# Performance work log

Measured on AMD Instinct MI355X. Metric: run time of the kernel, lower is better.

## Reference

```python
import jax, jax.numpy as jnp
import numpy as np

# static config (matches init_kwargs / chosen grid)
T, H, W = 8, 32, 32          # video token grid
WT, WH, WW = 4, 8, 8         # swin window
HEADS, HD = 16, 128
DIM = HEADS * HD             # 2048
LT = 256                     # text length
EPS = 1e-6
NT, NH, NW_ = T // WT, H // WH, W // WW
NWIN = NT * NH * NW_
WLEN = WT * WH * WW


def rmsnorm(x, g):
    # x: [..., HD], g: [HD]
    var = jnp.mean(x * x, axis=-1, keepdims=True)
    return x * jax.lax.rsqrt(var + EPS) * g


def setup_inputs() -> dict:
    key = jax.random.key(0)
    ks = jax.random.split(key, 8)
    s = 0.02
    Lv = T * H * W
    return {
        'vid': jax.random.normal(ks[0], (Lv, DIM), jnp.float32),
        'txt': jax.random.normal(ks[1], (LT, DIM), jnp.float32),
        'Wqkv_v': jax.random.normal(ks[2], (DIM, 3 * DIM), jnp.float32) * s,
        'bqkv_v': jnp.zeros((3 * DIM,), jnp.float32),
        'Wqkv_t': jax.random.normal(ks[3], (DIM, 3 * DIM), jnp.float32) * s,
        'bqkv_t': jnp.zeros((3 * DIM,), jnp.float32),
        'Wo_v': jax.random.normal(ks[4], (DIM, DIM), jnp.float32) * s,
        'bo_v': jnp.zeros((DIM,), jnp.float32),
        'Wo_t': jax.random.normal(ks[5], (DIM, DIM), jnp.float32) * s,
        'bo_t': jnp.zeros((DIM,), jnp.float32),
        'gq_v': jnp.ones((HD,), jnp.float32),
        'gk_v': jnp.ones((HD,), jnp.float32),
        'gq_t': jnp.ones((HD,), jnp.float32),
        'gk_t': jnp.ones((HD,), jnp.float32),
    }


def _forward(vid, txt, Wqkv_v, bqkv_v, Wqkv_t, bqkv_t, Wo_v, bo_v, Wo_t, bo_t,
             gq_v, gk_v, gq_t, gk_t):
    # per-modality QKV projections
    vqkv = vid @ Wqkv_v + bqkv_v                      # [Lv, 3*DIM]
    tqkv = txt @ Wqkv_t + bqkv_t                      # [LT, 3*DIM]
    # swin window partition: [T,H,W,C] -> [nWin, WLEN, 3, h, d]
    x = vqkv.reshape(NT, WT, NH, WH, NW_, WW, 3 * DIM)
    x = x.transpose(0, 2, 4, 1, 3, 5, 6).reshape(NWIN, WLEN, 3, HEADS, HD)
    vq, vk, vv = x[:, :, 0], x[:, :, 1], x[:, :, 2]
    t = tqkv.reshape(LT, 3, HEADS, HD)
    tq, tk, tv = t[:, 0], t[:, 1], t[:, 2]
    # QK norm (per-head RMSNorm with affine)
    vq, vk = rmsnorm(vq, gq_v), rmsnorm(vk, gk_v)
    tq, tk = rmsnorm(tq, gq_t), rmsnorm(tk, gk_t)
    # concat full text to every window (repeat_concat_idx)
    bt = lambda a: jnp.broadcast_to(a[None], (NWIN,) + a.shape)
    q = jnp.concatenate([vq, bt(tq)], axis=1)          # [nWin, S, h, d]
    k = jnp.concatenate([vk, bt(tk)], axis=1)
    v = jnp.concatenate([vv, bt(tv)], axis=1)
    # attention within each window (flash-varlen equivalent, equal lengths)
    scale = 1.0 / np.sqrt(HD).astype(np.float32)
    scores = jnp.einsum('nqhd,nkhd->nhqk', q, k) * scale
    p = jax.nn.softmax(scores, axis=-1)
    o = jnp.einsum('nhqk,nkhd->nqhd', p, v)            # [nWin, S, h, d]
    vo = o[:, :WLEN].reshape(NWIN, WLEN, DIM)
    to = o[:, WLEN:].mean(axis=0).reshape(LT, DIM)     # un-repeat text: mean over windows
    # window reverse -> flat [Lv, DIM]
    vo = vo.reshape(NT, NH, NW_, WT, WH, WW, DIM)
    vo = vo.transpose(0, 3, 1, 4, 2, 5, 6).reshape(T * H * W, DIM)
    return (vo @ Wo_v + bo_v, to @ Wo_t + bo_t)


def reference(vid, txt, Wqkv_v, bqkv_v, Wqkv_t, bqkv_t, Wo_v, bo_v, Wo_t, bo_t,
              gq_v, gk_v, gq_t, gk_t):
    return _forward(vid, txt, Wqkv_v, bqkv_v, Wqkv_t, bqkv_t, Wo_v, bo_v,
                    Wo_t, bo_t, gq_v, gk_v, gq_t, gk_t)
```

## Files before the change

### kernel.cpp

```cpp
#include <hip/hip_runtime.h>

typedef unsigned short u16;
typedef unsigned int   u32;
typedef __attribute__((ext_vector_type(8))) short short8;
typedef __attribute__((ext_vector_type(4))) float f32x4;

__device__ __forceinline__ u16 f2bf(float f) {
  union { float f; u32 u; } v; v.f = f;
  u32 r = v.u + 0x7fffu + ((v.u >> 16) & 1u);
  return (u16)(r >> 16);
}
__device__ __forceinline__ float bf2f(u32 bits) {
  union { u32 u; float f; } v; v.u = bits << 16; return v.f;
}
__device__ __forceinline__ void gl_lds16(const u16* g, u16* l) {
  __builtin_amdgcn_global_load_lds(
      (const __attribute__((address_space(1))) void*)g,
      (__attribute__((address_space(3))) void*)l, 16, 0, 0);
}

static constexpr int DIM  = 2048;
static constexpr int NQKV = 6144;

__global__ __launch_bounds__(256) void conv_f32_bf16(const float* __restrict__ in,
                                                     u16* __restrict__ out, int n4) {
  int id = blockIdx.x * 256 + threadIdx.x;
  if (id >= n4) return;
  float4 v = ((const float4*)in)[id];
  u32 lo = (u32)f2bf(v.x) | ((u32)f2bf(v.y) << 16);
  u32 hi = (u32)f2bf(v.z) | ((u32)f2bf(v.w) << 16);
  ((uint2*)out)[id] = make_uint2(lo, hi);
}

__global__ void tconv_kernel(const float* __restrict__ W, u16* __restrict__ Wt, int K, int N) {
  __shared__ float t[32][33];
  int tx = threadIdx.x, ty = threadIdx.y;
  int n0 = blockIdx.x * 32, k0 = blockIdx.y * 32;
  #pragma unroll
  for (int i = 0; i < 4; ++i)
    t[ty + i*8][tx] = W[(size_t)(k0 + ty + i*8) * N + n0 + tx];
  __syncthreads();
  #pragma unroll
  for (int i = 0; i < 4; ++i)
    Wt[(size_t)(n0 + ty + i*8) * K + k0 + tx] = f2bf(t[tx][ty + i*8]);
}

__global__ __launch_bounds__(256) void rms_kernel(u16* __restrict__ x,
                                                  const float* __restrict__ g, int nrows) {
  int w = threadIdx.x >> 6, lane = threadIdx.x & 63;
  int rid = blockIdx.x * 4 + w;
  if (rid >= nrows) return;
  u32* row = (u32*)x + (size_t)rid * 64;
  u32 u = row[lane];
  float f0 = bf2f(u & 0xffffu), f1 = bf2f(u >> 16);
  float s = f0*f0 + f1*f1;
  #pragma unroll
  for (int off = 1; off <= 32; off <<= 1) s += __shfl_xor(s, off);
  float r = rsqrtf(s * (1.0f/128.0f) + 1e-6f);
  float g0 = g[lane*2], g1 = g[lane*2+1];
  row[lane] = (u32)f2bf(f0*r*g0) | ((u32)f2bf(f1*r*g1) << 16);
}

__global__ __launch_bounds__(256)
void vtrans_kernel(const u16* __restrict__ src, u16* __restrict__ dst) {
  __shared__ u16 t[64][130];
  int nh = blockIdx.x, k0 = blockIdx.y * 64;
  const u16* s = src + ((size_t)nh*256 + k0)*128;
  u16* d = dst + (size_t)nh*128*256 + k0;
  int tid = threadIdx.x;
  #pragma unroll
  for (int it = 0; it < 4; ++it) {
    int c = tid + it*256;
    int row = c >> 4, ch = c & 15;
    short8 v = *(const short8*)(s + row*128 + ch*8);
    u32* dst32 = (u32*)&t[row][ch*8];
    const u32* v32 = (const u32*)&v;
    dst32[0] = v32[0]; dst32[1] = v32[1]; dst32[2] = v32[2]; dst32[3] = v32[3];
  }
  __syncthreads();
  #pragma unroll
  for (int it = 0; it < 4; ++it) {
    int c = tid + it*256;
    int dr = c >> 3, kg = c & 7;
    short8 v;
    #pragma unroll
    for (int j = 0; j < 8; ++j) v[j] = (short)t[kg*8+j][dr];
    *(short8*)(d + (size_t)dr*256 + kg*8) = v;
  }
}

template<int EPI>
__global__ __launch_bounds__(512, 2)
void gemm256(const u16* __restrict__ A, const u16* __restrict__ Bt,
             const float* __restrict__ bias,
             u16* __restrict__ o0, u16* __restrict__ o1, u16* __restrict__ o2,
             float* __restrict__ of, int ldo, int M, int N, int K)
{
  __shared__ __align__(16) u16 As[4][256*32];
  __shared__ __align__(16) u16 Bs[4][256*32];
  const int NT = K >> 5;
  int tid = threadIdx.x, lane = tid & 63, w = tid >> 6;
  int l15 = lane & 15, l4 = lane >> 4;
  int wm = w >> 2, wn = w & 3;

  int nbx = gridDim.x;
  int nwg = nbx * gridDim.y;
  int bid = blockIdx.y * nbx + blockIdx.x;
  int cpx = nwg >> 3;
  int swz = (bid & 7) * cpx + (bid >> 3);
  int n0 = (swz % nbx) * 256, m0 = (swz / nbx) * 256;

  int srow = tid >> 2, skc = (tid & 3) ^ ((tid >> 3) & 3);
  const u16* aS = A  + (size_t)(m0 + srow) * K + skc * 8;
  const u16* bS = Bt + (size_t)(n0 + srow) * K + skc * 8;
  const size_t halfStride = 128 * (size_t)K;
  const int ldsBase = w * 512;

  #define STAGE_A(slot, tt, half) \
    gl_lds16(aS + (size_t)(tt)*32 + (half)*halfStride, &As[slot][(half)*4096 + ldsBase])
  #define STAGE_B(slot, tt, half) \
    gl_lds16(bS + (size_t)(tt)*32 + (half)*halfStride, &Bs[slot][(half)*4096 + ldsBase])

  #pragma unroll
  for (int pt = 0; pt < 3; ++pt) {
    STAGE_A(pt, pt, 0); STAGE_A(pt, pt, 1);
    STAGE_B(pt, pt, 0); STAGE_B(pt, pt, 1);
  }
  asm volatile("s_waitcnt vmcnt(8)" ::: "memory");
  __builtin_amdgcn_s_barrier();

  f32x4 acc[8][4] = {};

  for (int t = 0; t < NT; ++t) {
    const u16* ab = As[t & 3];
    const u16* bb = Bs[t & 3];
    bool st = (t + 3 < NT);
    int slot = (t + 3) & 3;

    short8 bf_[4], af[4];
    #pragma unroll
    for (int j = 0; j < 4; ++j) {
      int rb = wn*64 + j*16 + l15;
      bf_[j] = *(const short8*)((const char*)bb + rb*64 + ((l4 ^ ((rb>>1)&3))*16));
    }
    #pragma unroll
    for (int i = 0; i < 4; ++i) {
      int ra = wm*128 + i*16 + l15;
      af[i] = *(const short8*)((const char*)ab + ra*64 + ((l4 ^ ((ra>>1)&3))*16));
    }
    if (st) { STAGE_A(slot, t+3, 0); STAGE_A(slot, t+3, 1); }
    __builtin_amdgcn_s_barrier();
    asm volatile("s_waitcnt lgkmcnt(0)" ::: "memory");
    __builtin_amdgcn_sched_barrier(0);
    __builtin_amdgcn_s_setprio(1);
    #pragma unroll
    for (int i = 0; i < 4; ++i)
      #pragma unroll
      for (int j = 0; j < 4; ++j)
        acc[i][j] = __builtin_amdgcn_mfma_f32_16x16x32_bf16(af[i], bf_[j], acc[i][j], 0, 0, 0);
    __builtin_amdgcn_s_setprio(0);
    __builtin_amdgcn_s_barrier();

    #pragma unroll
    for (int i = 0; i < 4; ++i) {
      int ra = wm*128 + 64 + i*16 + l15;
      af[i] = *(const short8*)((const char*)ab + ra*64 + ((l4 ^ ((ra>>1)&3))*16));
    }
    if (st) { STAGE_B(slot, t+3, 0); STAGE_B(slot, t+3, 1); }
    __builtin_amdgcn_s_barrier();
    asm volatile("s_waitcnt lgkmcnt(0)" ::: "memory");
    __builtin_amdgcn_sched_barrier(0);
    __builtin_amdgcn_s_setprio(1);
    #pragma unroll
    for (int i = 0; i < 4; ++i)
      #pragma unroll
      for (int j = 0; j < 4; ++j)
        acc[4+i][j] = __builtin_amdgcn_mfma_f32_16x16x32_bf16(af[i], bf_[j], acc[4+i][j], 0, 0, 0);
    __builtin_amdgcn_s_setprio(0);
    if (t <= NT - 4)      asm volatile("s_waitcnt vmcnt(8)" ::: "memory");
    else if (t == NT - 3) asm volatile("s_waitcnt vmcnt(4)" ::: "memory");
    else if (t == NT - 2) asm volatile("s_waitcnt vmcnt(0)" ::: "memory");
    __builtin_amdgcn_s_barrier();
  }
  #undef STAGE_A
  #undef STAGE_B

  #pragma unroll
  for (int i = 0; i < 8; ++i)
    #pragma unroll
    for (int j = 0; j < 4; ++j)
      #pragma unroll
      for (int r = 0; r < 4; ++r) {
        int m = m0 + wm*128 + i*16 + l4*4 + r;
        int n = n0 + wn*64  + j*16 + l15;
        float v = acc[i][j][r] + bias[n];
        if (EPI == 0) {
          int which = n >> 11, head = (n >> 7) & 15, d = n & 127;
          int t = m >> 10, hh = (m >> 5) & 31, ww = m & 31;
          int win = ((t>>2)<<4) + ((hh>>3)<<2) + (ww>>3);
          int p   = ((t&3)<<6) + ((hh&7)<<3) + (ww&7);
          u16* dst = which == 0 ? o0 : (which == 1 ? o1 : o2);
          dst[((size_t)(win*16 + head)*256 + p)*128 + d] = f2bf(v);
        } else {
          of[(size_t)m * ldo + n] = v;
        }
      }
}

template<int EPI>
__global__ __launch_bounds__(256)
void gemm128(const u16* __restrict__ A, const u16* __restrict__ Bt,
             const float* __restrict__ bias,
             u16* __restrict__ o0, u16* __restrict__ o1, u16* __restrict__ o2,
             float* __restrict__ of, int ldo, int M, int N, int K)
{
  __shared__ __align__(16) u16 As[128*32];
  __shared__ __align__(16) u16 Bs[128*32];
  int tid = threadIdx.x, lane = tid & 63, w = tid >> 6;
  int l15 = lane & 15, l4 = lane >> 4;
  int m0 = blockIdx.y * 128, n0 = blockIdx.x * 128;
  int wr = (w >> 1) * 64, wc = (w & 1) * 64;
  f32x4 acc[4][4] = {};

  int o0b = (w    )*1024 + lane*16;
  int o1b = (w + 4)*1024 + lane*16;
  int r0 = o0b >> 6, c0 = ((o0b >> 4) & 3) ^ ((r0 >> 1) & 3);
  int r1 = o1b >> 6, c1 = ((o1b >> 4) & 3) ^ ((r1 >> 1) & 3);
  const u16* a0 = A  + (size_t)(m0 + r0)*K + c0*8;
  const u16* a1 = A  + (size_t)(m0 + r1)*K + c1*8;
  const u16* b0 = Bt + (size_t)(n0 + r0)*K + c0*8;
  const u16* b1 = Bt + (size_t)(n0 + r1)*K + c1*8;
  u16* dA0 = As + (w    )*512;
  u16* dA1 = As + (w + 4)*512;
  u16* dB0 = Bs + (w    )*512;
  u16* dB1 = Bs + (w + 4)*512;

  for (int k0 = 0; k0 < K; k0 += 32) {
    gl_lds16(a0 + k0, dA0);
    gl_lds16(a1 + k0, dA1);
    gl_lds16(b0 + k0, dB0);
    gl_lds16(b1 + k0, dB1);
    __syncthreads();
    short8 af[4], bfr[4];
    #pragma unroll
    for (int t = 0; t < 4; ++t) {
      int ra = wr + t*16 + l15;
      af[t]  = *(const short8*)((const char*)As + ra*64 + ((l4 ^ ((ra>>1)&3))*16));
      int rb = wc + t*16 + l15;
      bfr[t] = *(const short8*)((const char*)Bs + rb*64 + ((l4 ^ ((rb>>1)&3))*16));
    }
    #pragma unroll
    for (int i = 0; i < 4; ++i)
      #pragma unroll
      for (int j = 0; j < 4; ++j)
        acc[i][j] = __builtin_amdgcn_mfma_f32_16x16x32_bf16(af[i], bfr[j], acc[i][j], 0, 0, 0);
    __syncthreads();
  }

  #pragma unroll
  for (int i = 0; i < 4; ++i)
    #pragma unroll
    for (int j = 0; j < 4; ++j)
      #pragma unroll
      for (int r = 0; r < 4; ++r) {
        int m = m0 + wr + i*16 + l4*4 + r;
        int n = n0 + wc + j*16 + l15;
        float v = acc[i][j][r] + bias[n];
        if (EPI == 1) {
          int which = n >> 11, head = (n >> 7) & 15, d = n & 127;
          u16* dst = which == 0 ? o0 : (which == 1 ? o1 : o2);
          dst[((size_t)head*256 + m)*128 + d] = f2bf(v);
        } else {
          of[(size_t)m * ldo + n] = v;
        }
      }
}

__global__ __launch_bounds__(512)
void attn_kernel(const u16* __restrict__ vq, const u16* __restrict__ vk, const u16* __restrict__ vv,
                 const u16* __restrict__ tq, const u16* __restrict__ tk, const u16* __restrict__ tv,
                 const float* __restrict__ gq_v, const float* __restrict__ gq_t,
                 u16* __restrict__ vo, float* __restrict__ to_acc)
{
  __shared__ __align__(16) u16 Ks[64*128];
  __shared__ __align__(16) u16 Vt[128*64];
  __shared__ __align__(16) u16 Ps[8][16*80];
  int tid = threadIdx.x, lane = tid & 63, w = tid >> 6;
  int l15 = lane & 15, l4 = lane >> 4;
  int bid = blockIdx.x;
  int logical = (bid & 7) * 256 + (bid >> 3);
  int nh_ = logical >> 2, qq = logical & 3;
  int h = nh_ & 15;
  int n = nh_ >> 4;
  int qt = qq * 128 + w * 16;

  const u16* Qb; const float* gq;
  if (qt < 256) { Qb = vq + ((size_t)nh_*256 + qt)*128; gq = gq_v; }
  else          { Qb = tq + ((size_t)h  *256 + (qt-256))*128; gq = gq_t; }
  short8 qf[4];
  float qv[4][8];
  float ss = 0.f;
  #pragma unroll
  for (int dt = 0; dt < 4; ++dt) {
    qf[dt] = *(const short8*)(Qb + l15*128 + l4*8 + dt*32);
    #pragma unroll
    for (int j = 0; j < 8; ++j) {
      float f = bf2f((u16)qf[dt][j]);
      qv[dt][j] = f; ss += f*f;
    }
  }
  ss += __shfl_xor(ss, 16); ss += __shfl_xor(ss, 32);
  float rr = rsqrtf(ss * (1.0f/128.0f) + 1e-6f);
  #pragma unroll
  for (int dt = 0; dt < 4; ++dt) {
    float4 g0 = *(const float4*)(gq + l4*8 + dt*32);
    float4 g1 = *(const float4*)(gq + l4*8 + dt*32 + 4);
    qf[dt][0] = (short)f2bf(qv[dt][0]*rr*g0.x); qf[dt][1] = (short)f2bf(qv[dt][1]*rr*g0.y);
    qf[dt][2] = (short)f2bf(qv[dt][2]*rr*g0.z); qf[dt][3] = (short)f2bf(qv[dt][3]*rr*g0.w);
    qf[dt][4] = (short)f2bf(qv[dt][4]*rr*g1.x); qf[dt][5] = (short)f2bf(qv[dt][5]*rr*g1.y);
    qf[dt][6] = (short)f2bf(qv[dt][6]*rr*g1.z); qf[dt][7] = (short)f2bf(qv[dt][7]*rr*g1.w);
  }

  int oK0 = w*1024 + lane*16, oK1 = oK0 + 8192;
  int kr0 = oK0 >> 8, kc0 = ((oK0 >> 4) & 15) ^ (kr0 & 7);
  int kr1 = oK1 >> 8, kc1 = ((oK1 >> 4) & 15) ^ (kr1 & 7);
  int vd0 = oK0 >> 7, vc0 = ((oK0 >> 4) & 7) ^ (vd0 & 7);
  int vd1 = oK1 >> 7, vc1 = ((oK1 >> 4) & 7) ^ (vd1 & 7);
  u16* KD0 = Ks + (w*1024)/2;  u16* KD1 = Ks + (w*1024 + 8192)/2;
  u16* VD0 = Vt + (w*1024)/2;  u16* VD1 = Vt + (w*1024 + 8192)/2;

  f32x4 o_[8] = {};
  float m_run[4] = {-1e30f,-1e30f,-1e30f,-1e30f};
  float l_run[4] = {0.f,0.f,0.f,0.f};
  const float scale = 0.08838834764831845f;
  u16* pb = Ps[w];

  for (int c = 0; c < 8; ++c) {
    int kb = c * 64;
    const u16* Kc; const u16* Vb; int vkb;
    if (kb < 256) { Kc = vk + ((size_t)nh_*256 + kb)*128; Vb = vv + (size_t)nh_*128*256; vkb = kb; }
    else          { Kc = tk + ((size_t)h  *256 + (kb-256))*128; Vb = tv + (size_t)h*128*256; vkb = kb - 256; }
    gl_lds16(Kc + kr0*128 + kc0*8, KD0);
    gl_lds16(Kc + kr1*128 + kc1*8, KD1);
    gl_lds16(Vb + (size_t)vd0*256 + vkb + vc0*8, VD0);
    gl_lds16(Vb + (size_t)vd1*256 + vkb + vc1*8, VD1);
    __syncthreads();

    f32x4 s4[4];
    __builtin_amdgcn_s_setprio(1);
    #pragma unroll
    for (int kt = 0; kt < 4; ++kt) {
      f32x4 sa = {0.f,0.f,0.f,0.f};
      int key = kt*16 + l15;
      #pragma unroll
      for (int dt = 0; dt < 4; ++dt) {
        int c16b = l4 + dt*4;
        short8 kf = *(const short8*)((const char*)Ks + key*256 + (((c16b ^ (key&7)))*16));
        sa = __builtin_amdgcn_mfma_f32_16x16x32_bf16(qf[dt], kf, sa, 0, 0, 0);
      }
      s4[kt] = sa;
    }
    __builtin_amdgcn_s_setprio(0);

    float f_[4];
    #pragma unroll
    for (int r = 0; r < 4; ++r) {
      float mx = fmaxf(fmaxf(s4[0][r], s4[1][r]), fmaxf(s4[2][r], s4[3][r])) * scale;
      #pragma unroll
      for (int off = 1; off <= 8; off <<= 1) mx = fmaxf(mx, __shfl_xor(mx, off));
      float nm = fmaxf(m_run[r], mx);
      f_[r] = __expf(m_run[r] - nm);
      m_run[r] = nm;
    }
    float p[4][4];
    #pragma unroll
    for (int kt = 0; kt < 4; ++kt)
      #pragma unroll
      for (int r = 0; r < 4; ++r)
        p[kt][r] = __expf(s4[kt][r]*scale - m_run[r]);
    #pragma unroll
    for (int r = 0; r < 4; ++r) {
      float sum = p[0][r] + p[1][r] + p[2][r] + p[3][r];
      #pragma unroll
      for (int off = 1; off <= 8; off <<= 1) sum += __shfl_xor(sum, off);
      l_run[r] = l_run[r]*f_[r] + sum;
    }
    #pragma unroll
    for (int dt = 0; dt < 8; ++dt) {
      f32x4 t = o_[dt];
      t[0]*=f_[0]; t[1]*=f_[1]; t[2]*=f_[2]; t[3]*=f_[3];
      o_[dt] = t;
    }

    #pragma unroll
    for (int kt = 0; kt < 4; ++kt)
      #pragma unroll
      for (int r = 0; r < 4; ++r)
        pb[(l4*4 + r)*80 + kt*16 + l15] = f2bf(p[kt][r]);
    #pragma unroll
    for (int ks = 0; ks < 2; ++ks) {
      short8 pa = *(const short8*)((const char*)pb + l15*160 + ks*64 + l4*16);
      __builtin_amdgcn_s_setprio(1);
      #pragma unroll
      for (int dt = 0; dt < 8; ++dt) {
        int d = dt*16 + l15;
        short8 vf = *(const short8*)((const char*)Vt + d*128 + (((ks*4 + l4) ^ (d&7))<<4));
        o_[dt] = __builtin_amdgcn_mfma_f32_16x16x32_bf16(pa, vf, o_[dt], 0, 0, 0);
      }
      __builtin_amdgcn_s_setprio(0);
    }
    __syncthreads();
  }

  float inv[4];
  #pragma unroll
  for (int r = 0; r < 4; ++r) inv[r] = 1.0f / l_run[r];
  int nt = n >> 4, nh2 = (n >> 2) & 3, nw = n & 3;
  #pragma unroll
  for (int dt = 0; dt < 8; ++dt) {
    int d = dt*16 + l15;
    int col = h*128 + d;
    #pragma unroll
    for (int r = 0; r < 4; ++r) {
      float val = o_[dt][r] * inv[r];
      int q = qt + l4*4 + r;
      if (q < 256) {
        int wt = q >> 6, wh = (q >> 3) & 7, ww = q & 7;
        int rg = ((nt*4 + wt)*32 + (nh2*8 + wh))*32 + (nw*8 + ww);
        vo[(size_t)rg*2048 + col] = f2bf(val);
      } else {
        atomicAdd(to_acc + (size_t)(q - 256)*2048 + col, val * (1.0f/32.0f));
      }
    }
  }
}

extern "C" void kernel_launch(void* const* d_in, const int* in_sizes, int n_in,
                              void* d_out, int out_size, void* d_ws, size_t ws_size,
                              hipStream_t stream) {
  const float* vid    = (const float*)d_in[0];
  const float* txt    = (const float*)d_in[1];
  const float* Wqkv_v = (const float*)d_in[2];
  const float* bqkv_v = (const float*)d_in[3];
  const float* Wqkv_t = (const float*)d_in[4];
  const float* bqkv_t = (const float*)d_in[5];
  const float* Wo_v   = (const float*)d_in[6];
  const float* bo_v   = (const float*)d_in[7];
  const float* Wo_t   = (const float*)d_in[8];
  const float* bo_t   = (const float*)d_in[9];
  const float* gq_v   = (const float*)d_in[10];
  const float* gk_v   = (const float*)d_in[11];
  const float* gq_t   = (const float*)d_in[12];
  const float* gk_t   = (const float*)d_in[13];
  float* out = (float*)d_out;

  char* p = (char*)d_ws;
  u16* vid_bf   = (u16*)p;  p += 8192ull*2048*2;
  u16* txt_bf   = (u16*)p;  p += 256ull*2048*2;
  u16* Wqkv_v_t = (u16*)p;  p += 6144ull*2048*2;
  u16* Wqkv_t_t = (u16*)p;  p += 6144ull*2048*2;
  u16* Wo_v_t   = (u16*)p;  p += 2048ull*2048*2;
  u16* Wo_t_t   = (u16*)p;  p += 2048ull*2048*2;
  u16* vq_w     = (u16*)p;  p += 32ull*16*256*128*2;
  u16* vk_w     = (u16*)p;  p += 32ull*16*256*128*2;
  u16* vv_w     = (u16*)p;  p += 32ull*16*256*128*2;
  u16* tq_w     = (u16*)p;  p += 16ull*256*128*2;
  u16* tk_w     = (u16*)p;  p += 16ull*256*128*2;
  u16* tv_w     = (u16*)p;  p += 16ull*256*128*2;
  u16* vo_pre   = (u16*)p;  p += 8192ull*2048*2;
  float* to_pre = (float*)p; p += 256ull*2048*4;
  u16* to_bf    = (u16*)p;  p += 256ull*2048*2;
  u16* vvT = vid_bf;
  u16* tvT = vid_bf + 512ull*128*256;

  hipMemsetAsync(to_pre, 0, 256ull*2048*4, stream);

  conv_f32_bf16<<<dim3(16384), dim3(256), 0, stream>>>(vid, vid_bf, 8192*2048/4);
  conv_f32_bf16<<<dim3(512),   dim3(256), 0, stream>>>(txt, txt_bf, 256*2048/4);
  tconv_kernel<<<dim3(192,64), dim3(32,8), 0, stream>>>(Wqkv_v, Wqkv_v_t, 2048, 6144);
  tconv_kernel<<<dim3(192,64), dim3(32,8), 0, stream>>>(Wqkv_t, Wqkv_t_t, 2048, 6144);
  tconv_kernel<<<dim3(64,64),  dim3(32,8), 0, stream>>>(Wo_v,   Wo_v_t,   2048, 2048);
  tconv_kernel<<<dim3(64,64),  dim3(32,8), 0, stream>>>(Wo_t,   Wo_t_t,   2048, 2048);

  gemm256<0><<<dim3(24,32), dim3(512), 0, stream>>>(vid_bf, Wqkv_v_t, bqkv_v,
      vq_w, vk_w, vv_w, nullptr, 0, 8192, NQKV, DIM);
  gemm128<1><<<dim3(48,2),  dim3(256), 0, stream>>>(txt_bf, Wqkv_t_t, bqkv_t,
      tq_w, tk_w, tv_w, nullptr, 0, 256, NQKV, DIM);

  vtrans_kernel<<<dim3(512,4), dim3(256), 0, stream>>>(vv_w, vvT);
  vtrans_kernel<<<dim3(16,4),  dim3(256), 0, stream>>>(tv_w, tvT);

  rms_kernel<<<dim3(32768), dim3(256), 0, stream>>>(vk_w, gk_v, 32*16*256);
  rms_kernel<<<dim3(1024),  dim3(256), 0, stream>>>(tk_w, gk_t, 16*256);

  attn_kernel<<<dim3(2048), dim3(512), 0, stream>>>(vq_w, vk_w, vvT, tq_w, tk_w, tvT,
                                                    gq_v, gq_t, vo_pre, to_pre);

  conv_f32_bf16<<<dim3(512), dim3(256), 0, stream>>>(to_pre, to_bf, 256*2048/4);

  gemm256<2><<<dim3(8,32), dim3(512), 0, stream>>>(vo_pre, Wo_v_t, bo_v,
      nullptr, nullptr, nullptr, out, 2048, 8192, 2048, 2048);
  gemm128<2><<<dim3(16,2), dim3(256), 0, stream>>>(to_bf, Wo_t_t, bo_t,
      nullptr, nullptr, nullptr, out + 16777216, 2048, 256, 2048, 2048);
}
```

Before: 639.4 us.

## Double-buffer attention K/V tiles and cut GEMM main-loop barriers

The attention kernel now double-buffers K/V chunks in LDS, prefetching the next chunk while computing the current one. The P staging buffer is removed and P is written into the current K buffer with a swizzled layout. Launch bounds request 4 blocks per CU. The GEMM main loop moves its vmcnt wait and barrier to the top of each iteration and drops the two intra-iteration barriers and lgkmcnt waits, which risks LDS read/write hazards when the prefetch slot is overwritten while other waves may still be reading it.

```diff
diff --git a/kernel.cpp b/kernel.cpp
--- a/kernel.cpp
+++ b/kernel.cpp
@@ -126,32 +126,35 @@
     STAGE_A(pt, pt, 0); STAGE_A(pt, pt, 1);
     STAGE_B(pt, pt, 0); STAGE_B(pt, pt, 1);
   }
-  asm volatile("s_waitcnt vmcnt(8)" ::: "memory");
-  __builtin_amdgcn_s_barrier();
 
   f32x4 acc[8][4] = {};
 
   for (int t = 0; t < NT; ++t) {
+    if (t < NT - 2)       asm volatile("s_waitcnt vmcnt(8)" ::: "memory");
+    else if (t == NT - 2) asm volatile("s_waitcnt vmcnt(4)" ::: "memory");
+    else                  asm volatile("s_waitcnt vmcnt(0)" ::: "memory");
+    __builtin_amdgcn_s_barrier();
+    asm volatile("" ::: "memory");
+
     const u16* ab = As[t & 3];
     const u16* bb = Bs[t & 3];
     bool st = (t + 3 < NT);
     int slot = (t + 3) & 3;
 
-    short8 bf_[4], af[4];
+    short8 bf_[4];
     #pragma unroll
     for (int j = 0; j < 4; ++j) {
       int rb = wn*64 + j*16 + l15;
       bf_[j] = *(const short8*)((const char*)bb + rb*64 + ((l4 ^ ((rb>>1)&3))*16));
     }
+
+    short8 af[4];
     #pragma unroll
     for (int i = 0; i < 4; ++i) {
       int ra = wm*128 + i*16 + l15;
       af[i] = *(const short8*)((const char*)ab + ra*64 + ((l4 ^ ((ra>>1)&3))*16));
     }
     if (st) { STAGE_A(slot, t+3, 0); STAGE_A(slot, t+3, 1); }
-    __builtin_amdgcn_s_barrier();
-    asm volatile("s_waitcnt lgkmcnt(0)" ::: "memory");
-    __builtin_amdgcn_sched_barrier(0);
     __builtin_amdgcn_s_setprio(1);
     #pragma unroll
     for (int i = 0; i < 4; ++i)
@@ -159,7 +162,6 @@
       for (int j = 0; j < 4; ++j)
         acc[i][j] = __builtin_amdgcn_mfma_f32_16x16x32_bf16(af[i], bf_[j], acc[i][j], 0, 0, 0);
     __builtin_amdgcn_s_setprio(0);
-    __builtin_amdgcn_s_barrier();
 
     #pragma unroll
     for (int i = 0; i < 4; ++i) {
@@ -167,9 +169,6 @@
       af[i] = *(const short8*)((const char*)ab + ra*64 + ((l4 ^ ((ra>>1)&3))*16));
     }
     if (st) { STAGE_B(slot, t+3, 0); STAGE_B(slot, t+3, 1); }
-    __builtin_amdgcn_s_barrier();
-    asm volatile("s_waitcnt lgkmcnt(0)" ::: "memory");
-    __builtin_amdgcn_sched_barrier(0);
     __builtin_amdgcn_s_setprio(1);
     #pragma unroll
     for (int i = 0; i < 4; ++i)
@@ -177,10 +176,6 @@
       for (int j = 0; j < 4; ++j)
         acc[4+i][j] = __builtin_amdgcn_mfma_f32_16x16x32_bf16(af[i], bf_[j], acc[4+i][j], 0, 0, 0);
     __builtin_amdgcn_s_setprio(0);
-    if (t <= NT - 4)      asm volatile("s_waitcnt vmcnt(8)" ::: "memory");
-    else if (t == NT - 3) asm volatile("s_waitcnt vmcnt(4)" ::: "memory");
-    else if (t == NT - 2) asm volatile("s_waitcnt vmcnt(0)" ::: "memory");
-    __builtin_amdgcn_s_barrier();
   }
   #undef STAGE_A
   #undef STAGE_B
@@ -276,15 +271,14 @@
       }
 }
 
-__global__ __launch_bounds__(512)
+__global__ __launch_bounds__(512, 4)
 void attn_kernel(const u16* __restrict__ vq, const u16* __restrict__ vk, const u16* __restrict__ vv,
                  const u16* __restrict__ tq, const u16* __restrict__ tk, const u16* __restrict__ tv,
                  const float* __restrict__ gq_v, const float* __restrict__ gq_t,
                  u16* __restrict__ vo, float* __restrict__ to_acc)
 {
-  __shared__ __align__(16) u16 Ks[64*128];
-  __shared__ __align__(16) u16 Vt[128*64];
-  __shared__ __align__(16) u16 Ps[8][16*80];
+  __shared__ __align__(16) u16 Ks[2*64*128];
+  __shared__ __align__(16) u16 Vt[2*128*64];
   int tid = threadIdx.x, lane = tid & 63, w = tid >> 6;
   int l15 = lane & 15, l4 = lane >> 4;
   int bid = blockIdx.x;
@@ -326,25 +320,37 @@
   int kr1 = oK1 >> 8, kc1 = ((oK1 >> 4) & 15) ^ (kr1 & 7);
   int vd0 = oK0 >> 7, vc0 = ((oK0 >> 4) & 7) ^ (vd0 & 7);
   int vd1 = oK1 >> 7, vc1 = ((oK1 >> 4) & 7) ^ (vd1 & 7);
-  u16* KD0 = Ks + (w*1024)/2;  u16* KD1 = Ks + (w*1024 + 8192)/2;
-  u16* VD0 = Vt + (w*1024)/2;  u16* VD1 = Vt + (w*1024 + 8192)/2;
 
   f32x4 o_[8] = {};
   float m_run[4] = {-1e30f,-1e30f,-1e30f,-1e30f};
   float l_run[4] = {0.f,0.f,0.f,0.f};
   const float scale = 0.08838834764831845f;
-  u16* pb = Ps[w];
+
+  #define STAGE_CHUNK(cc, buf)                                                        \
+    {                                                                                 \
+      int kb = (cc) * 64;                                                             \
+      const u16* Kc; const u16* Vb; int vkb;                                          \
+      if (kb < 256) { Kc = vk + ((size_t)nh_*256 + kb)*128;                           \
+                      Vb = vv + (size_t)nh_*128*256; vkb = kb; }                      \
+      else          { Kc = tk + ((size_t)h*256 + (kb-256))*128;                       \
+                      Vb = tv + (size_t)h*128*256; vkb = kb - 256; }                  \
+      gl_lds16(Kc + kr0*128 + kc0*8, Ks + (buf)*8192 + w*512);                        \
+      gl_lds16(Kc + kr1*128 + kc1*8, Ks + (buf)*8192 + w*512 + 4096);                 \
+      gl_lds16(Vb + (size_t)vd0*256 + vkb + vc0*8, Vt + (buf)*8192 + w*512);          \
+      gl_lds16(Vb + (size_t)vd1*256 + vkb + vc1*8, Vt + (buf)*8192 + w*512 + 4096);   \
+    }
+
+  STAGE_CHUNK(0, 0);
 
   for (int c = 0; c < 8; ++c) {
-    int kb = c * 64;
-    const u16* Kc; const u16* Vb; int vkb;
-    if (kb < 256) { Kc = vk + ((size_t)nh_*256 + kb)*128; Vb = vv + (size_t)nh_*128*256; vkb = kb; }
-    else          { Kc = tk + ((size_t)h  *256 + (kb-256))*128; Vb = tv + (size_t)h*128*256; vkb = kb - 256; }
-    gl_lds16(Kc + kr0*128 + kc0*8, KD0);
-    gl_lds16(Kc + kr1*128 + kc1*8, KD1);
-    gl_lds16(Vb + (size_t)vd0*256 + vkb + vc0*8, VD0);
-    gl_lds16(Vb + (size_t)vd1*256 + vkb + vc1*8, VD1);
-    __syncthreads();
+    int cur = c & 1;
+    __builtin_amdgcn_s_barrier();
+    if (c < 7) STAGE_CHUNK(c + 1, cur ^ 1);
+    if (c < 7) asm volatile("s_waitcnt vmcnt(4)" ::: "memory");
+    else       asm volatile("s_waitcnt vmcnt(0)" ::: "memory");
+    __builtin_amdgcn_s_barrier();
+    const char* KsB = (const char*)(Ks + cur*8192);
+    const char* VtB = (const char*)(Vt + cur*8192);
 
     f32x4 s4[4];
     __builtin_amdgcn_s_setprio(1);
@@ -355,7 +361,7 @@
       #pragma unroll
       for (int dt = 0; dt < 4; ++dt) {
         int c16b = l4 + dt*4;
-        short8 kf = *(const short8*)((const char*)Ks + key*256 + (((c16b ^ (key&7)))*16));
+        short8 kf = *(const short8*)(KsB + key*256 + (((c16b ^ (key&7)))*16));
         sa = __builtin_amdgcn_mfma_f32_16x16x32_bf16(qf[dt], kf, sa, 0, 0, 0);
       }
       s4[kt] = sa;
@@ -392,25 +398,29 @@
       o_[dt] = t;
     }
 
+    __builtin_amdgcn_s_barrier();
+    u16* pw = Ks + cur*8192 + w*1024;
     #pragma unroll
     for (int kt = 0; kt < 4; ++kt)
       #pragma unroll
-      for (int r = 0; r < 4; ++r)
-        pb[(l4*4 + r)*80 + kt*16 + l15] = f2bf(p[kt][r]);
+      for (int r = 0; r < 4; ++r) {
+        int q = l4*4 + r;
+        pw[q*64 + (((kt*2 + (l15>>3)) ^ (q&7))<<3) + (l15&7)] = f2bf(p[kt][r]);
+      }
     #pragma unroll
     for (int ks = 0; ks < 2; ++ks) {
-      short8 pa = *(const short8*)((const char*)pb + l15*160 + ks*64 + l4*16);
+      short8 pa = *(const short8*)((const char*)pw + l15*128 + (((ks*4 + l4) ^ (l15&7))<<4));
       __builtin_amdgcn_s_setprio(1);
       #pragma unroll
       for (int dt = 0; dt < 8; ++dt) {
         int d = dt*16 + l15;
-        short8 vf = *(const short8*)((const char*)Vt + d*128 + (((ks*4 + l4) ^ (d&7))<<4));
+        short8 vf = *(const short8*)(VtB + d*128 + (((ks*4 + l4) ^ (d&7))<<4));
         o_[dt] = __builtin_amdgcn_mfma_f32_16x16x32_bf16(pa, vf, o_[dt], 0, 0, 0);
       }
       __builtin_amdgcn_s_setprio(0);
     }
-    __syncthreads();
-  }
+  }
+  #undef STAGE_CHUNK
 
   float inv[4];
   #pragma unroll
```

Measured after the change: 644.3 us. Within noise of the previous version (+0.8%).
